# Performance work log

Hardware: AMD Instinct MI355X
Metric: run time of the kernel (lower is better)

Reference implementation:

```python
import jax, jax.numpy as jnp
import numpy as np

TEMPERATURE = 11.313708498984761  # sqrt(128)


def setup_inputs() -> dict:
    key = jax.random.key(0)
    k1, k2, k3 = jax.random.split(key, 3)
    B, N, D, Dv = 64, 8192, 128, 128
    q = jax.random.normal(k1, (B, D), dtype=jnp.float32)
    k = jax.random.normal(k2, (B, N, D), dtype=jnp.float32)
    v = jax.random.normal(k3, (B, N, Dv), dtype=jnp.float32)
    mask = jnp.zeros((B, N), dtype=bool)  # True = masked out
    return {"q": q, "k": k, "v": v, "mask": mask}


def reference(q, k, v, mask):
    # scores: (q[:,None,:] * k).sum(-1) / T  -> einsum 'bd,bnd->bn'
    attn = jnp.einsum('bd,bnd->bn', q, k) / TEMPERATURE
    attn = jnp.where(mask, -jnp.inf, attn)
    attn = jax.nn.softmax(attn, axis=1)  # [B, N]
    # output: (attn[:,:,None] * v).sum(1) -> einsum 'bn,bnd->bd'
    output = jnp.einsum('bn,bnd->bd', attn, v)
    return output, attn
```

## Files before the change

### kernel.cpp

```cpp
#include <hip/hip_runtime.h>
#include <math.h>

#define BATCH  64
#define NKEYS  8192
#define DIM    128
#define NCHUNK 64
#define CH     (NKEYS / NCHUNK)
static constexpr float SCALE = 0.08838834764831845f;

__global__ __launch_bounds__(256) void k_fused(
    const float* __restrict__ q, const float* __restrict__ k,
    const float* __restrict__ v, const unsigned char* __restrict__ mask,
    float* __restrict__ attn_raw, float* __restrict__ partO,
    float* __restrict__ mvals, float* __restrict__ lvals) {
    const int b  = blockIdx.x / NCHUNK;
    const int c  = blockIdx.x % NCHUNK;
    const int n0 = c * CH;
    const int tid  = threadIdx.x;
    const int wave = tid >> 6, lane = tid & 63, half = lane >> 5, l32 = lane & 31;

    __shared__ float sc[CH];
    __shared__ float red8[8];
    __shared__ float sm;
    __shared__ float red[8][DIM];

    const float4 qv = *reinterpret_cast<const float4*>(q + b * DIM + l32 * 4);
    const float* kb = k + (size_t)b * NKEYS * DIM;

    const int rw = wave * (CH / 4);
    for (int i = 0; i < CH / 8; ++i) {
        const int nl = rw + i * 2;
        const float4 kv = *reinterpret_cast<const float4*>(
            kb + (size_t)(n0 + nl) * DIM + lane * 4);
        float p = kv.x * qv.x + kv.y * qv.y + kv.z * qv.z + kv.w * qv.w;
        #pragma unroll
        for (int off = 16; off; off >>= 1) p += __shfl_down(p, off, 32);
        if (l32 == 0) {
            const int nn = nl + half;
            float s = p * SCALE;
            if (mask[(size_t)b * NKEYS + n0 + nn]) s = -__builtin_inff();
            sc[nn] = s;
            attn_raw[(size_t)b * NKEYS + n0 + nn] = s;
        }
    }
    __syncthreads();

    float mv = (tid < CH) ? sc[tid] : -__builtin_inff();
    #pragma unroll
    for (int off = 32; off; off >>= 1) mv = fmaxf(mv, __shfl_down(mv, off, 64));
    if (lane == 0) red8[wave] = mv;
    __syncthreads();
    if (tid == 0) sm = fmaxf(fmaxf(red8[0], red8[1]), fmaxf(red8[2], red8[3]));
    __syncthreads();
    const float m_c = sm;

    float e = 0.f;
    if (tid < CH) e = __expf(sc[tid] - m_c);
    float ls = e;
    #pragma unroll
    for (int off = 32; off; off >>= 1) ls += __shfl_down(ls, off, 64);
    if (lane == 0) red8[wave] = ls;
    if (tid < CH) sc[tid] = e;
    __syncthreads();
    if (tid == 0) {
        mvals[(size_t)b * NCHUNK + c] = m_c;
        lvals[(size_t)b * NCHUNK + c] = red8[0] + red8[1] + red8[2] + red8[3];
    }

    const int g = tid >> 5, d4 = (tid & 31) * 4;
    const float* vb = v + (size_t)b * NKEYS * DIM;
    float4 acc = {0.f, 0.f, 0.f, 0.f};
    for (int i = 0; i < CH; i += 8) {
        const int nl = i + g;
        const float w = sc[nl];
        const float4 vv = *reinterpret_cast<const float4*>(
            vb + (size_t)(n0 + nl) * DIM + d4);
        acc.x += w * vv.x; acc.y += w * vv.y; acc.z += w * vv.z; acc.w += w * vv.w;
    }
    *reinterpret_cast<float4*>(&red[g][d4]) = acc;
    __syncthreads();
    if (tid < DIM) {
        float s = 0.f;
        #pragma unroll
        for (int gg = 0; gg < 8; ++gg) s += red[gg][tid];
        partO[((size_t)b * NCHUNK + c) * DIM + tid] = s;
    }
}

__global__ __launch_bounds__(256) void k_finish(
    const float* __restrict__ partO, const float* __restrict__ mvals,
    const float* __restrict__ lvals, float* __restrict__ out,
    float* __restrict__ Mb, float* __restrict__ Li) {
    const int b = blockIdx.x;
    const int tid = threadIdx.x;
    __shared__ float scl[NCHUNK];
    __shared__ float sLi;
    if (tid < 64) {
        const float m = mvals[(size_t)b * NCHUNK + tid];
        float mm = m;
        #pragma unroll
        for (int off = 32; off; off >>= 1) mm = fmaxf(mm, __shfl_down(mm, off, 64));
        mm = __shfl(mm, 0, 64);
        const float s = __expf(m - mm);
        scl[tid] = s;
        float lc = lvals[(size_t)b * NCHUNK + tid] * s;
        #pragma unroll
        for (int off = 32; off; off >>= 1) lc += __shfl_down(lc, off, 64);
        if (tid == 0) {
            const float li = 1.0f / lc;
            sLi = li; Mb[b] = mm; Li[b] = li;
        }
    }
    __syncthreads();
    if (tid < DIM) {
        float s = 0.f;
        for (int c = 0; c < NCHUNK; ++c)
            s += partO[((size_t)b * NCHUNK + c) * DIM + tid] * scl[c];
        out[b * DIM + tid] = s * sLi;
    }
}

__global__ __launch_bounds__(256) void k_norm(
    float* __restrict__ attn, const float* __restrict__ Mb,
    const float* __restrict__ Li) {
    const size_t i4 = (size_t)blockIdx.x * blockDim.x + threadIdx.x;
    const size_t base = i4 * 4;
    const int b = (int)(base >> 13);
    const float m = Mb[b], li = Li[b];
    float4 s = *reinterpret_cast<float4*>(attn + base);
    s.x = __expf(s.x - m) * li;
    s.y = __expf(s.y - m) * li;
    s.z = __expf(s.z - m) * li;
    s.w = __expf(s.w - m) * li;
    *reinterpret_cast<float4*>(attn + base) = s;
}

extern "C" void kernel_launch(void* const* d_in, const int* in_sizes, int n_in,
                              void* d_out, int out_size, void* d_ws, size_t ws_size,
                              hipStream_t stream) {
    const float* q = (const float*)d_in[0];
    const float* k = (const float*)d_in[1];
    const float* v = (const float*)d_in[2];
    const unsigned char* mask = (const unsigned char*)d_in[3];

    float* out  = (float*)d_out;
    float* attn = out + BATCH * DIM;

    float* partO = (float*)d_ws;
    float* mvals = partO + (size_t)BATCH * NCHUNK * DIM;
    float* lvals = mvals + BATCH * NCHUNK;
    float* Mb    = lvals + BATCH * NCHUNK;
    float* Li    = Mb + BATCH;

    k_fused <<<dim3(BATCH * NCHUNK), dim3(256), 0, stream>>>(
        q, k, v, mask, attn, partO, mvals, lvals);
    k_finish<<<dim3(BATCH), dim3(256), 0, stream>>>(
        partO, mvals, lvals, out, Mb, Li);
    k_norm  <<<dim3(BATCH * NKEYS / (256 * 4)), dim3(256), 0, stream>>>(
        attn, Mb, Li);
}
```

Measured before the change: 119.8 us.

## Prefetch V into registers early and store chunk-local exp weights for rescaling

```diff
diff --git a/kernel.cpp b/kernel.cpp
--- a/kernel.cpp
+++ b/kernel.cpp
@@ -5,13 +5,13 @@
 #define NKEYS  8192
 #define DIM    128
 #define NCHUNK 64
-#define CH     (NKEYS / NCHUNK)
+#define CH     128
 static constexpr float SCALE = 0.08838834764831845f;
 
-__global__ __launch_bounds__(256) void k_fused(
+__global__ __launch_bounds__(256, 3) void k_fused(
     const float* __restrict__ q, const float* __restrict__ k,
     const float* __restrict__ v, const unsigned char* __restrict__ mask,
-    float* __restrict__ attn_raw, float* __restrict__ partO,
+    float* __restrict__ attn_e, float* __restrict__ partO,
     float* __restrict__ mvals, float* __restrict__ lvals) {
     const int b  = blockIdx.x / NCHUNK;
     const int c  = blockIdx.x % NCHUNK;
@@ -20,118 +20,125 @@
     const int wave = tid >> 6, lane = tid & 63, half = lane >> 5, l32 = lane & 31;
 
     __shared__ float sc[CH];
-    __shared__ float red8[8];
-    __shared__ float sm;
+    __shared__ float redm[4];
+    __shared__ float redl[4];
     __shared__ float red[8][DIM];
 
-    const float4 qv = *reinterpret_cast<const float4*>(q + b * DIM + l32 * 4);
+    const int g = tid >> 5, d4 = (tid & 31) * 4;
+    const float* vb = v + (size_t)b * NKEYS * DIM;
+    float4 vreg[16];
+    #pragma unroll
+    for (int i = 0; i < 16; ++i)
+        vreg[i] = *reinterpret_cast<const float4*>(
+            vb + (size_t)(n0 + i * 8 + g) * DIM + d4);
+
+    float4 qv = *reinterpret_cast<const float4*>(q + b * DIM + l32 * 4);
+    qv.x *= SCALE; qv.y *= SCALE; qv.z *= SCALE; qv.w *= SCALE;
     const float* kb = k + (size_t)b * NKEYS * DIM;
-
-    const int rw = wave * (CH / 4);
-    for (int i = 0; i < CH / 8; ++i) {
+    const int rw = wave * 32;
+    #pragma unroll
+    for (int i = 0; i < 16; ++i) {
         const int nl = rw + i * 2;
         const float4 kv = *reinterpret_cast<const float4*>(
             kb + (size_t)(n0 + nl) * DIM + lane * 4);
         float p = kv.x * qv.x + kv.y * qv.y + kv.z * qv.z + kv.w * qv.w;
         #pragma unroll
         for (int off = 16; off; off >>= 1) p += __shfl_down(p, off, 32);
-        if (l32 == 0) {
-            const int nn = nl + half;
-            float s = p * SCALE;
-            if (mask[(size_t)b * NKEYS + n0 + nn]) s = -__builtin_inff();
-            sc[nn] = s;
-            attn_raw[(size_t)b * NKEYS + n0 + nn] = s;
-        }
+        if (l32 == 0) sc[nl + half] = p;
     }
     __syncthreads();
 
-    float mv = (tid < CH) ? sc[tid] : -__builtin_inff();
+    float s = -__builtin_inff();
+    if (tid < CH) {
+        s = sc[tid];
+        if (mask[(size_t)b * NKEYS + n0 + tid]) s = -__builtin_inff();
+    }
+    float mv = s;
     #pragma unroll
     for (int off = 32; off; off >>= 1) mv = fmaxf(mv, __shfl_down(mv, off, 64));
-    if (lane == 0) red8[wave] = mv;
+    if (lane == 0) redm[wave] = mv;
     __syncthreads();
-    if (tid == 0) sm = fmaxf(fmaxf(red8[0], red8[1]), fmaxf(red8[2], red8[3]));
-    __syncthreads();
-    const float m_c = sm;
+    const float m_c = fmaxf(fmaxf(redm[0], redm[1]), fmaxf(redm[2], redm[3]));
 
     float e = 0.f;
-    if (tid < CH) e = __expf(sc[tid] - m_c);
+    if (tid < CH) {
+        e = __expf(s - m_c);
+        sc[tid] = e;
+        attn_e[(size_t)b * NKEYS + n0 + tid] = e;
+    }
     float ls = e;
     #pragma unroll
     for (int off = 32; off; off >>= 1) ls += __shfl_down(ls, off, 64);
-    if (lane == 0) red8[wave] = ls;
-    if (tid < CH) sc[tid] = e;
+    if (lane == 0) redl[wave] = ls;
     __syncthreads();
     if (tid == 0) {
         mvals[(size_t)b * NCHUNK + c] = m_c;
-        lvals[(size_t)b * NCHUNK + c] = red8[0] + red8[1] + red8[2] + red8[3];
+        lvals[(size_t)b * NCHUNK + c] = redl[0] + redl[1] + redl[2] + redl[3];
     }
 
-    const int g = tid >> 5, d4 = (tid & 31) * 4;
-    const float* vb = v + (size_t)b * NKEYS * DIM;
     float4 acc = {0.f, 0.f, 0.f, 0.f};
-    for (int i = 0; i < CH; i += 8) {
-        const int nl = i + g;
-        const float w = sc[nl];
-        const float4 vv = *reinterpret_cast<const float4*>(
-            vb + (size_t)(n0 + nl) * DIM + d4);
-        acc.x += w * vv.x; acc.y += w * vv.y; acc.z += w * vv.z; acc.w += w * vv.w;
+    #pragma unroll
+    for (int i = 0; i < 16; ++i) {
+        const float w = sc[i * 8 + g];
+        acc.x += w * vreg[i].x; acc.y += w * vreg[i].y;
+        acc.z += w * vreg[i].z; acc.w += w * vreg[i].w;
     }
     *reinterpret_cast<float4*>(&red[g][d4]) = acc;
     __syncthreads();
     if (tid < DIM) {
-        float s = 0.f;
+        float o = 0.f;
         #pragma unroll
-        for (int gg = 0; gg < 8; ++gg) s += red[gg][tid];
-        partO[((size_t)b * NCHUNK + c) * DIM + tid] = s;
+        for (int gg = 0; gg < 8; ++gg) o += red[gg][tid];
+        partO[((size_t)b * NCHUNK + c) * DIM + tid] = o;
     }
 }
 
 __global__ __launch_bounds__(256) void k_finish(
     const float* __restrict__ partO, const float* __restrict__ mvals,
     const float* __restrict__ lvals, float* __restrict__ out,
-    float* __restrict__ Mb, float* __restrict__ Li) {
+    float* __restrict__ cscale) {
     const int b = blockIdx.x;
     const int tid = threadIdx.x;
     __shared__ float scl[NCHUNK];
     __shared__ float sLi;
+    __shared__ float oh[DIM];
     if (tid < 64) {
         const float m = mvals[(size_t)b * NCHUNK + tid];
         float mm = m;
         #pragma unroll
         for (int off = 32; off; off >>= 1) mm = fmaxf(mm, __shfl_down(mm, off, 64));
         mm = __shfl(mm, 0, 64);
-        const float s = __expf(m - mm);
-        scl[tid] = s;
-        float lc = lvals[(size_t)b * NCHUNK + tid] * s;
+        const float sc_ = __expf(m - mm);
+        scl[tid] = sc_;
+        float lc = lvals[(size_t)b * NCHUNK + tid] * sc_;
         #pragma unroll
         for (int off = 32; off; off >>= 1) lc += __shfl_down(lc, off, 64);
-        if (tid == 0) {
-            const float li = 1.0f / lc;
-            sLi = li; Mb[b] = mm; Li[b] = li;
-        }
+        if (tid == 0) sLi = 1.0f / lc;
     }
     __syncthreads();
-    if (tid < DIM) {
-        float s = 0.f;
-        for (int c = 0; c < NCHUNK; ++c)
-            s += partO[((size_t)b * NCHUNK + c) * DIM + tid] * scl[c];
-        out[b * DIM + tid] = s * sLi;
-    }
+    const float Li = sLi;
+    if (tid < 64) cscale[(size_t)b * NCHUNK + tid] = scl[tid] * Li;
+
+    const int d = tid & 127;
+    const int c0 = (tid >> 7) * 32;
+    const float* pb = partO + (size_t)b * NCHUNK * DIM;
+    float o = 0.f;
+    #pragma unroll 4
+    for (int c = c0; c < c0 + 32; ++c) o += pb[c * DIM + d] * scl[c];
+    if (tid >= 128) oh[d] = o;
+    __syncthreads();
+    if (tid < 128) out[b * DIM + d] = (o + oh[d]) * Li;
 }
 
 __global__ __launch_bounds__(256) void k_norm(
-    float* __restrict__ attn, const float* __restrict__ Mb,
-    const float* __restrict__ Li) {
+    float* __restrict__ attn, const float* __restrict__ cscale) {
     const size_t i4 = (size_t)blockIdx.x * blockDim.x + threadIdx.x;
     const size_t base = i4 * 4;
     const int b = (int)(base >> 13);
-    const float m = Mb[b], li = Li[b];
+    const int cl = (int)((base >> 7) & (NCHUNK - 1));
+    const float scl_ = cscale[(size_t)b * NCHUNK + cl];
     float4 s = *reinterpret_cast<float4*>(attn + base);
-    s.x = __expf(s.x - m) * li;
-    s.y = __expf(s.y - m) * li;
-    s.z = __expf(s.z - m) * li;
-    s.w = __expf(s.w - m) * li;
+    s.x *= scl_; s.y *= scl_; s.z *= scl_; s.w *= scl_;
     *reinterpret_cast<float4*>(attn + base) = s;
 }
 
@@ -146,16 +153,15 @@
     float* out  = (float*)d_out;
     float* attn = out + BATCH * DIM;
 
-    float* partO = (float*)d_ws;
-    float* mvals = partO + (size_t)BATCH * NCHUNK * DIM;
-    float* lvals = mvals + BATCH * NCHUNK;
-    float* Mb    = lvals + BATCH * NCHUNK;
-    float* Li    = Mb + BATCH;
+    float* partO  = (float*)d_ws;
+    float* mvals  = partO + (size_t)BATCH * NCHUNK * DIM;
+    float* lvals  = mvals + BATCH * NCHUNK;
+    float* cscale = lvals + BATCH * NCHUNK;
 
     k_fused <<<dim3(BATCH * NCHUNK), dim3(256), 0, stream>>>(
         q, k, v, mask, attn, partO, mvals, lvals);
     k_finish<<<dim3(BATCH), dim3(256), 0, stream>>>(
-        partO, mvals, lvals, out, Mb, Li);
+        partO, mvals, lvals, out, cscale);
     k_norm  <<<dim3(BATCH * NKEYS / (256 * 4)), dim3(256), 0, stream>>>(
-        attn, Mb, Li);
+        attn, cscale);
 }
```

After: 112.1 us. 1.07x faster.
